# Kernel tuning notes

Measured on AMD Instinct MI355X. Metric: run time of the kernel, lower is better.

The kernel has to match this reference:

```python
import jax, jax.numpy as jnp
import numpy as np

HEAD_QK_SIZE = 256
VOCAB_SIZE = 32000


def setup_inputs() -> dict:
    key = jax.random.key(0)
    k1, k2, k3, k4 = jax.random.split(key, 4)
    T, C, D = 4096, 1024, HEAD_QK_SIZE
    x = jax.random.normal(k1, (T, C), dtype=jnp.float32)
    idx = jax.random.randint(k2, (T,), 0, VOCAB_SIZE, dtype=jnp.int64)
    # Dense kernels (no bias), scaled like default lecun init magnitude
    Wq = jax.random.normal(k3, (C, D), dtype=jnp.float32) / np.sqrt(C)
    Wk = jax.random.normal(k4, (C, D), dtype=jnp.float32) / np.sqrt(C)
    return {"x": x, "idx": idx, "Wq": Wq, "Wk": Wk}


def reference(x, idx, Wq, Wk):
    # x: [T, C], idx: [T]
    T = x.shape[0]
    q = x @ Wq  # [T, D]
    k = x @ Wk  # [T, D]
    c = (q @ k.T) * (1.0 / HEAD_QK_SIZE)  # [T, T]
    causal = jnp.tril(jnp.ones((T, T), dtype=bool))
    c = jnp.where(causal, c, jnp.zeros((), dtype=c.dtype))
    # c @ one_hot(idx, vocab) == scatter-add of c's columns into vocab slots
    out = jax.ops.segment_sum(c.T, idx, num_segments=VOCAB_SIZE).T  # [T, vocab]
    return out
```

## Files before the change

### kernel.cpp

```cpp
#include <hip/hip_runtime.h>
#include <math.h>

constexpr int T = 4096;
constexpr int C = 1024;
constexpr int D = 256;
constexpr int VOCAB = 32000;
constexpr int VHALF = VOCAB / 2;
constexpr int NT = T / 64;
constexpr int NTILES = NT * (NT + 1) / 2;

typedef __attribute__((ext_vector_type(8))) short bf16x8;
typedef __attribute__((ext_vector_type(4))) float f32x4;

__device__ inline unsigned short f2bf(float f) {
    union { float f; unsigned int u; } v; v.f = f;
    unsigned int u = v.u + 0x7FFFu + ((v.u >> 16) & 1u);
    return (unsigned short)(u >> 16);
}

__global__ __launch_bounds__(256) void convert_x_kernel(
    const float* __restrict__ x, unsigned short* __restrict__ xb)
{
    const int i = (blockIdx.x * 256 + threadIdx.x) * 8;
    float4 a = *(const float4*)(x + i);
    float4 b = *(const float4*)(x + i + 4);
    union { bf16x8 v; unsigned short s[8]; } o;
    o.s[0] = f2bf(a.x); o.s[1] = f2bf(a.y); o.s[2] = f2bf(a.z); o.s[3] = f2bf(a.w);
    o.s[4] = f2bf(b.x); o.s[5] = f2bf(b.y); o.s[6] = f2bf(b.z); o.s[7] = f2bf(b.w);
    *(bf16x8*)(xb + i) = o.v;
}

__global__ __launch_bounds__(256) void transpose_w_kernel(
    const float* __restrict__ Wq, const float* __restrict__ Wk,
    unsigned short* __restrict__ WT)
{
    const float* W = blockIdx.z ? Wk : Wq;
    const int k0 = blockIdx.x * 64, n0 = blockIdx.y * 64;
    __shared__ float tile[64][65];
    const int tid = threadIdx.x;
    #pragma unroll
    for (int p = 0; p < 16; ++p) {
        const int e = p * 256 + tid;
        const int r = e >> 6, c = e & 63;
        tile[c][r] = W[(size_t)(k0 + r) * D + n0 + c];
    }
    __syncthreads();
    #pragma unroll
    for (int p = 0; p < 2; ++p) {
        const int e = p * 256 + tid;
        const int rr = e >> 3, cc = e & 7;
        union { bf16x8 v; unsigned short s[8]; } o;
        #pragma unroll
        for (int i = 0; i < 8; ++i) o.s[i] = f2bf(tile[rr][cc * 8 + i]);
        *(bf16x8*)(WT + (size_t)(blockIdx.z * D + n0 + rr) * C + k0 + cc * 8) = o.v;
    }
}

__global__ __launch_bounds__(256) void qk_mfma_kernel(
    const unsigned short* __restrict__ xb,
    const unsigned short* __restrict__ WT,
    unsigned short* __restrict__ qk)
{
    const int m0 = blockIdx.x * 64, n0 = blockIdx.y * 64;
    __shared__ __align__(16) unsigned short As[64 * 64];
    __shared__ __align__(16) unsigned short Bs[64 * 64];
    const int tid = threadIdx.x;
    const int wave = tid >> 6, lane = tid & 63;
    const int quad = lane >> 4, lr = lane & 15;
    const int wm = wave >> 1, wn = wave & 1;

    f32x4 acc[2][2] = {};

    for (int k0 = 0; k0 < C; k0 += 64) {
        #pragma unroll
        for (int p = 0; p < 2; ++p) {
            const int e = p * 256 + tid;
            const int r = e >> 3, c = e & 7, cs = c ^ (r & 7);
            *(bf16x8*)(As + r * 64 + cs * 8) =
                *(const bf16x8*)(xb + (size_t)(m0 + r) * C + k0 + c * 8);
            *(bf16x8*)(Bs + r * 64 + cs * 8) =
                *(const bf16x8*)(WT + (size_t)(n0 + r) * C + k0 + c * 8);
        }
        __syncthreads();
        #pragma unroll
        for (int kk = 0; kk < 64; kk += 32) {
            bf16x8 a[2], b[2];
            #pragma unroll
            for (int s = 0; s < 2; ++s) {
                const int ra = wm * 32 + s * 16 + lr;
                const int ca = ((kk >> 3) + quad) ^ (ra & 7);
                a[s] = *(const bf16x8*)(As + ra * 64 + ca * 8);
                const int rb = wn * 32 + s * 16 + lr;
                const int cb = ((kk >> 3) + quad) ^ (rb & 7);
                b[s] = *(const bf16x8*)(Bs + rb * 64 + cb * 8);
            }
            #pragma unroll
            for (int i = 0; i < 2; ++i)
                #pragma unroll
                for (int j = 0; j < 2; ++j)
                    acc[i][j] = __builtin_amdgcn_mfma_f32_16x16x32_bf16(
                        a[i], b[j], acc[i][j], 0, 0, 0);
        }
        __syncthreads();
    }

    #pragma unroll
    for (int i = 0; i < 2; ++i)
        #pragma unroll
        for (int j = 0; j < 2; ++j)
            #pragma unroll
            for (int r = 0; r < 4; ++r) {
                const int row = m0 + wm * 32 + i * 16 + quad * 4 + r;
                const int col = n0 + wn * 32 + j * 16 + lr;
                qk[(size_t)row * 512 + col] = f2bf(acc[i][j][r]);
            }
}

__global__ __launch_bounds__(256) void qkt_mfma_kernel(
    const unsigned short* __restrict__ qk,
    float* __restrict__ c_ws)
{
    const int bid = blockIdx.x;
    int ti = (int)((sqrtf(8.0f * (float)bid + 1.0f) - 1.0f) * 0.5f);
    while ((ti + 1) * (ti + 2) / 2 <= bid) ++ti;
    while (ti * (ti + 1) / 2 > bid) --ti;
    const int tj = bid - ti * (ti + 1) / 2;

    __shared__ __align__(16) unsigned short As[64 * 64];
    __shared__ __align__(16) unsigned short Bs[64 * 64];
    const int tid = threadIdx.x;
    const int wave = tid >> 6, lane = tid & 63;
    const int quad = lane >> 4, lr = lane & 15;
    const int wm = wave >> 1, wn = wave & 1;

    f32x4 acc[2][2] = {};

    const unsigned short* qp = qk + (size_t)ti * 64 * 512;
    const unsigned short* kp = qk + (size_t)tj * 64 * 512 + 256;

    for (int k0 = 0; k0 < D; k0 += 64) {
        #pragma unroll
        for (int p = 0; p < 2; ++p) {
            const int e = p * 256 + tid;
            const int r = e >> 3, c = e & 7, cs = c ^ (r & 7);
            *(bf16x8*)(As + r * 64 + cs * 8) =
                *(const bf16x8*)(qp + (size_t)r * 512 + k0 + c * 8);
            *(bf16x8*)(Bs + r * 64 + cs * 8) =
                *(const bf16x8*)(kp + (size_t)r * 512 + k0 + c * 8);
        }
        __syncthreads();
        #pragma unroll
        for (int kk = 0; kk < 64; kk += 32) {
            bf16x8 a[2], b[2];
            #pragma unroll
            for (int s = 0; s < 2; ++s) {
                const int ra = wm * 32 + s * 16 + lr;
                const int ca = ((kk >> 3) + quad) ^ (ra & 7);
                a[s] = *(const bf16x8*)(As + ra * 64 + ca * 8);
                const int rb = wn * 32 + s * 16 + lr;
                const int cb = ((kk >> 3) + quad) ^ (rb & 7);
                b[s] = *(const bf16x8*)(Bs + rb * 64 + cb * 8);
            }
            #pragma unroll
            for (int i = 0; i < 2; ++i)
                #pragma unroll
                for (int j = 0; j < 2; ++j)
                    acc[i][j] = __builtin_amdgcn_mfma_f32_16x16x32_bf16(
                        a[i], b[j], acc[i][j], 0, 0, 0);
        }
        __syncthreads();
    }

    const float scale = 1.0f / 256.0f;
    float* tile = c_ws + (size_t)bid * 4096;
    #pragma unroll
    for (int i = 0; i < 2; ++i)
        #pragma unroll
        for (int j = 0; j < 2; ++j)
            #pragma unroll
            for (int r = 0; r < 4; ++r) {
                const int row = wm * 32 + i * 16 + quad * 4 + r;
                const int col = wn * 32 + j * 16 + lr;
                const int rg = ti * 64 + row, cg = tj * 64 + col;
                tile[row * 64 + col] = (cg <= rg) ? acc[i][j][r] * scale : 0.0f;
            }
}

__global__ __launch_bounds__(1024) void row_scatter_kernel(
    const float* __restrict__ c_ws,
    const int* __restrict__ idx,
    float* __restrict__ out)
{
    __shared__ float4 hist4[VHALF / 4];
    float* hist = (float*)hist4;

    const int t  = blockIdx.x;
    const int lo = blockIdx.y * VHALF;
    const int tid = threadIdx.x;

    const float4 z4 = {0.0f, 0.0f, 0.0f, 0.0f};
    for (int v = tid; v < VHALF / 4; v += 1024) hist4[v] = z4;
    __syncthreads();

    const int ti = t >> 6;
    const int il = t & 63;
    const int jmax = (ti + 1) * 64;
    const size_t row_base = (size_t)ti * (ti + 1) / 2;

    const int j4 = tid * 4;
    if (j4 < jmax) {
        const int tj = j4 >> 6, jl = j4 & 63;
        const float4 vv = *(const float4*)(c_ws + (row_base + tj) * 4096 + il * 64 + jl);
        const int4  iv = *(const int4*)(idx + j4);
        int v0 = iv.x - lo, v1 = iv.y - lo, v2 = iv.z - lo, v3 = iv.w - lo;
        if ((unsigned)v0 < (unsigned)VHALF && vv.x != 0.0f) atomicAdd(&hist[v0], vv.x);
        if ((unsigned)v1 < (unsigned)VHALF && vv.y != 0.0f) atomicAdd(&hist[v1], vv.y);
        if ((unsigned)v2 < (unsigned)VHALF && vv.z != 0.0f) atomicAdd(&hist[v2], vv.z);
        if ((unsigned)v3 < (unsigned)VHALF && vv.w != 0.0f) atomicAdd(&hist[v3], vv.w);
    }
    __syncthreads();

    float4* orow = (float4*)(out + (size_t)t * VOCAB + lo);
    for (int v = tid; v < VHALF / 4; v += 1024) orow[v] = hist4[v];
}

extern "C" void kernel_launch(void* const* d_in, const int* in_sizes, int n_in,
                              void* d_out, int out_size, void* d_ws, size_t ws_size,
                              hipStream_t stream)
{
    const float* x   = (const float*)d_in[0];
    const int*   idx = (const int*)d_in[1];
    const float* Wq  = (const float*)d_in[2];
    const float* Wk  = (const float*)d_in[3];
    float* out = (float*)d_out;

    unsigned short* xb = (unsigned short*)d_ws;
    unsigned short* WT = xb + (size_t)T * C;
    unsigned short* qk = WT + (size_t)2 * D * C;
    float* c_ws = (float*)(qk + (size_t)T * 2 * D);

    convert_x_kernel<<<dim3((T * C) / (256 * 8)), 256, 0, stream>>>(x, xb);
    transpose_w_kernel<<<dim3(C / 64, D / 64, 2), 256, 0, stream>>>(Wq, Wk, WT);
    qk_mfma_kernel<<<dim3(T / 64, (2 * D) / 64), 256, 0, stream>>>(xb, WT, qk);
    qkt_mfma_kernel<<<dim3(NTILES), 256, 0, stream>>>(qk, c_ws);
    row_scatter_kernel<<<dim3(T, 2), 1024, 0, stream>>>(c_ws, idx, out);
}
```

Measured before the change: 587.0 us.

## Pack causal scores as bf16 rows, split vocab in quarters, fuse prep kernels

```diff
diff --git a/kernel.cpp b/kernel.cpp
--- a/kernel.cpp
+++ b/kernel.cpp
@@ -5,7 +5,7 @@
 constexpr int C = 1024;
 constexpr int D = 256;
 constexpr int VOCAB = 32000;
-constexpr int VHALF = VOCAB / 2;
+constexpr int VQ = VOCAB / 4;
 constexpr int NT = T / 64;
 constexpr int NTILES = NT * (NT + 1) / 2;
 
@@ -17,42 +17,54 @@
     unsigned int u = v.u + 0x7FFFu + ((v.u >> 16) & 1u);
     return (unsigned short)(u >> 16);
 }
-
-__global__ __launch_bounds__(256) void convert_x_kernel(
-    const float* __restrict__ x, unsigned short* __restrict__ xb)
-{
-    const int i = (blockIdx.x * 256 + threadIdx.x) * 8;
-    float4 a = *(const float4*)(x + i);
-    float4 b = *(const float4*)(x + i + 4);
-    union { bf16x8 v; unsigned short s[8]; } o;
-    o.s[0] = f2bf(a.x); o.s[1] = f2bf(a.y); o.s[2] = f2bf(a.z); o.s[3] = f2bf(a.w);
-    o.s[4] = f2bf(b.x); o.s[5] = f2bf(b.y); o.s[6] = f2bf(b.z); o.s[7] = f2bf(b.w);
-    *(bf16x8*)(xb + i) = o.v;
-}
-
-__global__ __launch_bounds__(256) void transpose_w_kernel(
+__device__ inline float bf2f(unsigned short s) {
+    union { unsigned int u; float f; } v; v.u = ((unsigned int)s) << 16;
+    return v.f;
+}
+__device__ inline void gl_lds16(const unsigned short* g, unsigned short* l) {
+    __builtin_amdgcn_global_load_lds(
+        (const __attribute__((address_space(1))) unsigned int*)g,
+        (__attribute__((address_space(3))) unsigned int*)l, 16, 0, 0);
+}
+
+__global__ __launch_bounds__(256) void prep_kernel(
+    const float* __restrict__ x,
     const float* __restrict__ Wq, const float* __restrict__ Wk,
-    unsigned short* __restrict__ WT)
-{
-    const float* W = blockIdx.z ? Wk : Wq;
-    const int k0 = blockIdx.x * 64, n0 = blockIdx.y * 64;
-    __shared__ float tile[64][65];
-    const int tid = threadIdx.x;
-    #pragma unroll
-    for (int p = 0; p < 16; ++p) {
-        const int e = p * 256 + tid;
-        const int r = e >> 6, c = e & 63;
-        tile[c][r] = W[(size_t)(k0 + r) * D + n0 + c];
-    }
-    __syncthreads();
-    #pragma unroll
-    for (int p = 0; p < 2; ++p) {
-        const int e = p * 256 + tid;
-        const int rr = e >> 3, cc = e & 7;
+    unsigned short* __restrict__ xb, unsigned short* __restrict__ WT)
+{
+    const int tid = threadIdx.x;
+    if (blockIdx.x < 2048) {
+        const int i = (blockIdx.x * 256 + tid) * 8;
+        float4 a = *(const float4*)(x + i);
+        float4 b = *(const float4*)(x + i + 4);
         union { bf16x8 v; unsigned short s[8]; } o;
-        #pragma unroll
-        for (int i = 0; i < 8; ++i) o.s[i] = f2bf(tile[rr][cc * 8 + i]);
-        *(bf16x8*)(WT + (size_t)(blockIdx.z * D + n0 + rr) * C + k0 + cc * 8) = o.v;
+        o.s[0] = f2bf(a.x); o.s[1] = f2bf(a.y); o.s[2] = f2bf(a.z); o.s[3] = f2bf(a.w);
+        o.s[4] = f2bf(b.x); o.s[5] = f2bf(b.y); o.s[6] = f2bf(b.z); o.s[7] = f2bf(b.w);
+        *(bf16x8*)(xb + i) = o.v;
+    } else {
+        const int bid = blockIdx.x - 2048;
+        const int w  = bid >> 6;
+        const int rem = bid & 63;
+        const int k0 = (rem >> 2) * 64;
+        const int n0 = (rem & 3) * 64;
+        const float* W = w ? Wk : Wq;
+        __shared__ float tile[64][65];
+        #pragma unroll
+        for (int p = 0; p < 16; ++p) {
+            const int e = p * 256 + tid;
+            const int r = e >> 6, c = e & 63;
+            tile[c][r] = W[(size_t)(k0 + r) * D + n0 + c];
+        }
+        __syncthreads();
+        #pragma unroll
+        for (int p = 0; p < 2; ++p) {
+            const int e = p * 256 + tid;
+            const int rr = e >> 3, cc = e & 7;
+            union { bf16x8 v; unsigned short s[8]; } o;
+            #pragma unroll
+            for (int i = 0; i < 8; ++i) o.s[i] = f2bf(tile[rr][cc * 8 + i]);
+            *(bf16x8*)(WT + (size_t)(w * D + n0 + rr) * C + k0 + cc * 8) = o.v;
+        }
     }
 }
 
@@ -68,18 +80,17 @@
     const int wave = tid >> 6, lane = tid & 63;
     const int quad = lane >> 4, lr = lane & 15;
     const int wm = wave >> 1, wn = wave & 1;
+    const int rsub = lane >> 3, c8 = (lane & 7) * 8;
 
     f32x4 acc[2][2] = {};
 
     for (int k0 = 0; k0 < C; k0 += 64) {
         #pragma unroll
-        for (int p = 0; p < 2; ++p) {
-            const int e = p * 256 + tid;
-            const int r = e >> 3, c = e & 7, cs = c ^ (r & 7);
-            *(bf16x8*)(As + r * 64 + cs * 8) =
-                *(const bf16x8*)(xb + (size_t)(m0 + r) * C + k0 + c * 8);
-            *(bf16x8*)(Bs + r * 64 + cs * 8) =
-                *(const bf16x8*)(WT + (size_t)(n0 + r) * C + k0 + c * 8);
+        for (int q = 0; q < 2; ++q) {
+            const int ch = wave * 2 + q;
+            const int r = ch * 8 + rsub;
+            gl_lds16(xb + (size_t)(m0 + r) * C + k0 + c8, As + ch * 512);
+            gl_lds16(WT + (size_t)(n0 + r) * C + k0 + c8, Bs + ch * 512);
         }
         __syncthreads();
         #pragma unroll
@@ -87,12 +98,8 @@
             bf16x8 a[2], b[2];
             #pragma unroll
             for (int s = 0; s < 2; ++s) {
-                const int ra = wm * 32 + s * 16 + lr;
-                const int ca = ((kk >> 3) + quad) ^ (ra & 7);
-                a[s] = *(const bf16x8*)(As + ra * 64 + ca * 8);
-                const int rb = wn * 32 + s * 16 + lr;
-                const int cb = ((kk >> 3) + quad) ^ (rb & 7);
-                b[s] = *(const bf16x8*)(Bs + rb * 64 + cb * 8);
+                a[s] = *(const bf16x8*)(As + (wm * 32 + s * 16 + lr) * 64 + kk + quad * 8);
+                b[s] = *(const bf16x8*)(Bs + (wn * 32 + s * 16 + lr) * 64 + kk + quad * 8);
             }
             #pragma unroll
             for (int i = 0; i < 2; ++i)
@@ -118,7 +125,7 @@
 
 __global__ __launch_bounds__(256) void qkt_mfma_kernel(
     const unsigned short* __restrict__ qk,
-    float* __restrict__ c_ws)
+    unsigned short* __restrict__ cpack)
 {
     const int bid = blockIdx.x;
     int ti = (int)((sqrtf(8.0f * (float)bid + 1.0f) - 1.0f) * 0.5f);
@@ -132,6 +139,7 @@
     const int wave = tid >> 6, lane = tid & 63;
     const int quad = lane >> 4, lr = lane & 15;
     const int wm = wave >> 1, wn = wave & 1;
+    const int rsub = lane >> 3, c8 = (lane & 7) * 8;
 
     f32x4 acc[2][2] = {};
 
@@ -140,13 +148,11 @@
 
     for (int k0 = 0; k0 < D; k0 += 64) {
         #pragma unroll
-        for (int p = 0; p < 2; ++p) {
-            const int e = p * 256 + tid;
-            const int r = e >> 3, c = e & 7, cs = c ^ (r & 7);
-            *(bf16x8*)(As + r * 64 + cs * 8) =
-                *(const bf16x8*)(qp + (size_t)r * 512 + k0 + c * 8);
-            *(bf16x8*)(Bs + r * 64 + cs * 8) =
-                *(const bf16x8*)(kp + (size_t)r * 512 + k0 + c * 8);
+        for (int q = 0; q < 2; ++q) {
+            const int ch = wave * 2 + q;
+            const int r = ch * 8 + rsub;
+            gl_lds16(qp + (size_t)r * 512 + k0 + c8, As + ch * 512);
+            gl_lds16(kp + (size_t)r * 512 + k0 + c8, Bs + ch * 512);
         }
         __syncthreads();
         #pragma unroll
@@ -154,12 +160,8 @@
             bf16x8 a[2], b[2];
             #pragma unroll
             for (int s = 0; s < 2; ++s) {
-                const int ra = wm * 32 + s * 16 + lr;
-                const int ca = ((kk >> 3) + quad) ^ (ra & 7);
-                a[s] = *(const bf16x8*)(As + ra * 64 + ca * 8);
-                const int rb = wn * 32 + s * 16 + lr;
-                const int cb = ((kk >> 3) + quad) ^ (rb & 7);
-                b[s] = *(const bf16x8*)(Bs + rb * 64 + cb * 8);
+                a[s] = *(const bf16x8*)(As + (wm * 32 + s * 16 + lr) * 64 + kk + quad * 8);
+                b[s] = *(const bf16x8*)(Bs + (wn * 32 + s * 16 + lr) * 64 + kk + quad * 8);
             }
             #pragma unroll
             for (int i = 0; i < 2; ++i)
@@ -172,7 +174,7 @@
     }
 
     const float scale = 1.0f / 256.0f;
-    float* tile = c_ws + (size_t)bid * 4096;
+    unsigned short* Cs = As;
     #pragma unroll
     for (int i = 0; i < 2; ++i)
         #pragma unroll
@@ -182,46 +184,63 @@
                 const int row = wm * 32 + i * 16 + quad * 4 + r;
                 const int col = wn * 32 + j * 16 + lr;
                 const int rg = ti * 64 + row, cg = tj * 64 + col;
-                tile[row * 64 + col] = (cg <= rg) ? acc[i][j][r] * scale : 0.0f;
-            }
-}
-
-__global__ __launch_bounds__(1024) void row_scatter_kernel(
-    const float* __restrict__ c_ws,
+                Cs[row * 64 + col] = f2bf((cg <= rg) ? acc[i][j][r] * scale : 0.0f);
+            }
+    __syncthreads();
+
+    const size_t tbase = (size_t)4096 * ((size_t)ti * (ti + 1) / 2);
+    const int len = (ti + 1) * 64;
+    #pragma unroll
+    for (int p = 0; p < 2; ++p) {
+        const int cidx = p * 256 + tid;
+        const int row = cidx >> 3, o8 = (cidx & 7) * 8;
+        *(bf16x8*)(cpack + tbase + (size_t)row * len + tj * 64 + o8) =
+            *(const bf16x8*)(Cs + row * 64 + o8);
+    }
+}
+
+__global__ __launch_bounds__(256) void row_scatter_kernel(
+    const unsigned short* __restrict__ cpack,
     const int* __restrict__ idx,
     float* __restrict__ out)
 {
-    __shared__ float4 hist4[VHALF / 4];
+    __shared__ f32x4 hist4[VQ / 4];
     float* hist = (float*)hist4;
 
     const int t  = blockIdx.x;
-    const int lo = blockIdx.y * VHALF;
-    const int tid = threadIdx.x;
-
-    const float4 z4 = {0.0f, 0.0f, 0.0f, 0.0f};
-    for (int v = tid; v < VHALF / 4; v += 1024) hist4[v] = z4;
+    const int lo = blockIdx.y * VQ;
+    const int tid = threadIdx.x;
+
+    const f32x4 z4 = {0.0f, 0.0f, 0.0f, 0.0f};
+    for (int v = tid; v < VQ / 4; v += 256) hist4[v] = z4;
     __syncthreads();
 
-    const int ti = t >> 6;
-    const int il = t & 63;
-    const int jmax = (ti + 1) * 64;
-    const size_t row_base = (size_t)ti * (ti + 1) / 2;
-
-    const int j4 = tid * 4;
-    if (j4 < jmax) {
-        const int tj = j4 >> 6, jl = j4 & 63;
-        const float4 vv = *(const float4*)(c_ws + (row_base + tj) * 4096 + il * 64 + jl);
-        const int4  iv = *(const int4*)(idx + j4);
-        int v0 = iv.x - lo, v1 = iv.y - lo, v2 = iv.z - lo, v3 = iv.w - lo;
-        if ((unsigned)v0 < (unsigned)VHALF && vv.x != 0.0f) atomicAdd(&hist[v0], vv.x);
-        if ((unsigned)v1 < (unsigned)VHALF && vv.y != 0.0f) atomicAdd(&hist[v1], vv.y);
-        if ((unsigned)v2 < (unsigned)VHALF && vv.z != 0.0f) atomicAdd(&hist[v2], vv.z);
-        if ((unsigned)v3 < (unsigned)VHALF && vv.w != 0.0f) atomicAdd(&hist[v3], vv.w);
+    const int ti = t >> 6, il = t & 63;
+    const int len = (ti + 1) * 64;
+    const unsigned short* rowp =
+        cpack + (size_t)4096 * ((size_t)ti * (ti + 1) / 2) + (size_t)il * len;
+    const int nch = len >> 3;
+
+    for (int ch = tid; ch < nch; ch += 256) {
+        union { bf16x8 v; unsigned short s[8]; } cv;
+        cv.v = *(const bf16x8*)(rowp + ch * 8);
+        union { int4 a[2]; int j[8]; } ji;
+        ji.a[0] = *(const int4*)(idx + ch * 8);
+        ji.a[1] = *(const int4*)(idx + ch * 8 + 4);
+        #pragma unroll
+        for (int i = 0; i < 8; ++i) {
+            const int v = ji.j[i] - lo;
+            if ((unsigned)v < (unsigned)VQ) {
+                const float f = bf2f(cv.s[i]);
+                if (f != 0.0f) atomicAdd(&hist[v], f);
+            }
+        }
     }
     __syncthreads();
 
-    float4* orow = (float4*)(out + (size_t)t * VOCAB + lo);
-    for (int v = tid; v < VHALF / 4; v += 1024) orow[v] = hist4[v];
+    f32x4* orow = (f32x4*)(out + (size_t)t * VOCAB + lo);
+    for (int v = tid; v < VQ / 4; v += 256)
+        __builtin_nontemporal_store(hist4[v], orow + v);
 }
 
 extern "C" void kernel_launch(void* const* d_in, const int* in_sizes, int n_in,
@@ -237,11 +256,10 @@
     unsigned short* xb = (unsigned short*)d_ws;
     unsigned short* WT = xb + (size_t)T * C;
     unsigned short* qk = WT + (size_t)2 * D * C;
-    float* c_ws = (float*)(qk + (size_t)T * 2 * D);
-
-    convert_x_kernel<<<dim3((T * C) / (256 * 8)), 256, 0, stream>>>(x, xb);
-    transpose_w_kernel<<<dim3(C / 64, D / 64, 2), 256, 0, stream>>>(Wq, Wk, WT);
+    unsigned short* cpack = qk + (size_t)T * 2 * D;
+
+    prep_kernel<<<dim3(2048 + 128), 256, 0, stream>>>(x, Wq, Wk, xb, WT);
     qk_mfma_kernel<<<dim3(T / 64, (2 * D) / 64), 256, 0, stream>>>(xb, WT, qk);
-    qkt_mfma_kernel<<<dim3(NTILES), 256, 0, stream>>>(qk, c_ws);
-    row_scatter_kernel<<<dim3(T, 2), 1024, 0, stream>>>(c_ws, idx, out);
-}
+    qkt_mfma_kernel<<<dim3(NTILES), 256, 0, stream>>>(qk, cpack);
+    row_scatter_kernel<<<dim3(T, 4), 256, 0, stream>>>(cpack, idx, out);
+}
```

Measured after the change: 564.2 us. 1.04x faster.
